# Performance work log

Hardware: AMD Instinct MI355X
Metric: run time of the kernel (lower is better)

Reference implementation:

```python
import jax, jax.numpy as jnp
import numpy as np

H, D_MODEL, DK, DV = 16, 1024, 64, 64
B, S = 4, 2048
LN_EPS = 1e-6
NEG = -1e9


def setup_inputs() -> dict:
    key = jax.random.key(0)
    ks = jax.random.split(key, 8)
    query = jax.random.normal(ks[0], (B, S, D_MODEL), dtype=jnp.float32)
    k_in = jax.random.normal(ks[1], (B, S, D_MODEL), dtype=jnp.float32)
    v_in = jax.random.normal(ks[2], (B, S, D_MODEL), dtype=jnp.float32)
    mask = jax.random.randint(ks[3], (B, S, S), 0, 2, dtype=jnp.int32)
    sc = 1.0 / np.sqrt(D_MODEL)
    w_qs = jax.random.normal(ks[4], (D_MODEL, H * DK), dtype=jnp.float32) * sc
    w_ks = jax.random.normal(ks[5], (D_MODEL, H * DK), dtype=jnp.float32) * sc
    w_vs = jax.random.normal(ks[6], (D_MODEL, H * DV), dtype=jnp.float32) * sc
    w_out = jax.random.normal(ks[7], (H * DV, D_MODEL), dtype=jnp.float32) * (1.0 / np.sqrt(H * DV))
    ln_g = jnp.ones((D_MODEL,), dtype=jnp.float32)
    ln_b = jnp.zeros((D_MODEL,), dtype=jnp.float32)
    return {"query": query, "key": k_in, "value": v_in, "mask": mask,
            "w_qs": w_qs, "w_ks": w_ks, "w_vs": w_vs, "w_out": w_out,
            "ln_g": ln_g, "ln_b": ln_b}


def reference(query, key, value, mask, w_qs, w_ks, w_vs, w_out, ln_g, ln_b):
    # projections -> [B, H, S, dk/dv]
    q = (query @ w_qs).reshape(B, S, H, DK).transpose(0, 2, 1, 3)
    k = (key @ w_ks).reshape(B, S, H, DK).transpose(0, 2, 1, 3)
    v = (value @ w_vs).reshape(B, S, H, DV).transpose(0, 2, 1, 3)
    scores = jnp.einsum('bhqd,bhkd->bhqk', q, k) / np.sqrt(DK)
    scores = jnp.where(mask[:, None, :, :] == 0, NEG, scores)
    p = jax.nn.softmax(scores, axis=-1)  # dropout = identity in eval
    x = jnp.einsum('bhqk,bhkd->bhqd', p, v)  # [B,H,S,DV]
    x = x.transpose(0, 2, 1, 3).reshape(B, S, H * DV)
    out = x @ w_out + query  # dropout identity, residual
    mu = out.mean(-1, keepdims=True)
    var = out.var(-1, keepdims=True)
    return (out - mu) / jnp.sqrt(var + LN_EPS) * ln_g + ln_b
```

## Files before the change

### kernel.cpp

```cpp
#include <hip/hip_runtime.h>

#define BB   4
#define SS   2048
#define HH   16
#define DM   1024
#define DKV  64
#define LNEPS 1e-6f

#define MD_BF16 0
#define MD_F32  1
#define MD_F16  2

typedef __attribute__((ext_vector_type(8))) short bf16x8;
typedef __attribute__((ext_vector_type(4))) float f32x4;
#define MFMA16(a,b,c) __builtin_amdgcn_mfma_f32_16x16x32_bf16(a,b,c,0,0,0)

__device__ __forceinline__ void gl_lds16(const ushort* g, ushort* l) {
    __builtin_amdgcn_global_load_lds(
        (const __attribute__((address_space(1))) void*)g,
        (__attribute__((address_space(3))) void*)l, 16, 0, 0);
}
__device__ __forceinline__ void wait_vm0_barrier() {
    asm volatile("s_waitcnt vmcnt(0)" ::: "memory");
    __builtin_amdgcn_s_barrier();
}

__device__ __forceinline__ float2 unpack2(unsigned int u) {
    union { unsigned int i; float f; } a, b;
    a.i = u << 16;
    b.i = u & 0xffff0000u;
    return make_float2(a.f, b.f);
}
__device__ __forceinline__ unsigned short f2bf(float f) {
    union { float f; unsigned int i; } c; c.f = f;
    unsigned int u = c.i;
    unsigned int r = u + 0x7fffu + ((u >> 16) & 1u);
    return (unsigned short)(r >> 16);
}
__device__ __forceinline__ unsigned short f2bf_t(float f) {
    union { float f; unsigned int i; } c; c.f = f;
    return (unsigned short)(c.i >> 16);
}
__device__ __forceinline__ float h2f(unsigned int bits16) {
    unsigned short s = (unsigned short)bits16;
    _Float16 x;
    __builtin_memcpy(&x, &s, 2);
    return (float)x;
}
__device__ __forceinline__ void load8m(const void* p, int mode, size_t e0, float* o) {
    if (mode == MD_F32) {
        const float* f = (const float*)p + e0;
        float4 a = *(const float4*)f;
        float4 b = *(const float4*)(f + 4);
        o[0] = a.x; o[1] = a.y; o[2] = a.z; o[3] = a.w;
        o[4] = b.x; o[5] = b.y; o[6] = b.z; o[7] = b.w;
    } else {
        uint4 u = *(const uint4*)((const ushort*)p + e0);
        unsigned v[4] = {u.x, u.y, u.z, u.w};
        if (mode == MD_BF16) {
#pragma unroll
            for (int j = 0; j < 4; ++j) { float2 t = unpack2(v[j]); o[2*j] = t.x; o[2*j+1] = t.y; }
        } else {
#pragma unroll
            for (int j = 0; j < 4; ++j) { o[2*j] = h2f(v[j] & 0xFFFFu); o[2*j+1] = h2f(v[j] >> 16); }
        }
    }
}
__device__ __forceinline__ void load4m(const void* p, int mode, size_t e0, float* o) {
    if (mode == MD_F32) {
        float4 v = *(const float4*)((const float*)p + e0);
        o[0] = v.x; o[1] = v.y; o[2] = v.z; o[3] = v.w;
    } else {
        uint2 u = *(const uint2*)((const ushort*)p + e0);
        if (mode == MD_BF16) {
            float2 a = unpack2(u.x), b = unpack2(u.y);
            o[0] = a.x; o[1] = a.y; o[2] = b.x; o[3] = b.y;
        } else {
            o[0] = h2f(u.x & 0xFFFFu); o[1] = h2f(u.x >> 16);
            o[2] = h2f(u.y & 0xFFFFu); o[3] = h2f(u.y >> 16);
        }
    }
}
__device__ __forceinline__ float loadS(const void* p, int mode, size_t i) {
    if (mode == MD_F32) return ((const float*)p)[i];
    unsigned short u = ((const ushort*)p)[i];
    if (mode == MD_BF16) { union { unsigned i; float f; } c; c.i = (unsigned)u << 16; return c.f; }
    return h2f(u);
}

struct SniffArgs { const void* p[10]; int nhalf[10]; };

__global__ void sniff_all(SniffArgs a, int* __restrict__ modes) {
    __shared__ int cE, cO;
    const int slots[9] = {0, 1, 2, 4, 5, 6, 7, 8, 9};
    const int slot = slots[blockIdx.x];
    const ushort* p = (const ushort*)a.p[slot];
    const int nhalf = a.nhalf[slot];
    if (threadIdx.x == 0) { cE = 0; cO = 0; }
    __syncthreads();
    int e = 0, o = 0;
    for (int i = threadIdx.x; i < nhalf; i += 256) {
        unsigned ex = (p[i] >> 7) & 0xFFu;
        int hit = (ex < 100u || ex == 0xFFu) ? 1 : 0;
        if (i & 1) o += hit; else e += hit;
    }
    atomicAdd(&cE, e);
    atomicAdd(&cO, o);
    __syncthreads();
    if (threadIdx.x == 0) {
        int total = cE + cO;
        modes[slot] = (total < 48) ? MD_BF16 : ((cO * 4 < cE) ? MD_F32 : MD_F16);
    }
}

__global__ __launch_bounds__(256) void mpack(
    const int* __restrict__ mask, unsigned int* __restrict__ pm)
{
    const int w = blockIdx.x * 256 + threadIdx.x;
    const int* p = mask + (size_t)w * 32;
    unsigned int bits = 0u;
#pragma unroll
    for (int j = 0; j < 8; ++j) {
        int4 v = *(const int4*)(p + j * 4);
        bits |= (v.x ? 1u : 0u) << (4 * j);
        bits |= (v.y ? 1u : 0u) << (4 * j + 1);
        bits |= (v.z ? 1u : 0u) << (4 * j + 2);
        bits |= (v.w ? 1u : 0u) << (4 * j + 3);
    }
    pm[w] = bits;
}

__global__ __launch_bounds__(256) void aconv(
    const void* __restrict__ A, ushort* __restrict__ Ab,
    const int* __restrict__ modes, int slot)
{
    const int m = modes[slot];
    const size_t e0 = ((size_t)blockIdx.x * 256 + threadIdx.x) * 16;
    float t[16];
    load8m(A, m, e0, t);
    load8m(A, m, e0 + 8, t + 8);
    union { ushort u[16]; uint4 v[2]; } p;
#pragma unroll
    for (int j = 0; j < 16; ++j) p.u[j] = f2bf(t[j]);
    *(uint4*)&Ab[e0]     = p.v[0];
    *(uint4*)&Ab[e0 + 8] = p.v[1];
}

struct WtArgs { const void* W[3]; ushort* Wt[3]; int slot[3]; };

__device__ __forceinline__ void wtrans_body(
    const void* __restrict__ W, ushort* __restrict__ Wt, int m)
{
    __shared__ ushort T[64][68];
    const int tid = threadIdx.x;
    const int k0 = blockIdx.y * 64, n0 = blockIdx.x * 64;

    const int r = tid >> 2, c = (tid & 3) * 16;
    float t[4];
#pragma unroll
    for (int j = 0; j < 4; ++j) {
        load4m(W, m, (size_t)(k0 + r) * DM + n0 + c + 4 * j, t);
#pragma unroll
        for (int i = 0; i < 4; ++i) T[r][c + 4 * j + i] = f2bf(t[i]);
    }
    __syncthreads();

    const int rn = tid >> 2, ck = (tid & 3) * 16;
    union { ushort u[8]; uint4 v; } p0, p1;
#pragma unroll
    for (int j = 0; j < 8; ++j) { p0.u[j] = T[ck + j][rn]; p1.u[j] = T[ck + 8 + j][rn]; }
    ushort* op = &Wt[(size_t)(n0 + rn) * DM + k0 + ck];
    *(uint4*)op = p0.v;
    *(uint4*)(op + 8) = p1.v;
}

__global__ __launch_bounds__(256) void wtrans3(WtArgs a, const int* __restrict__ modes) {
    const int g = blockIdx.z;
    wtrans_body(a.W[g], a.Wt[g], modes[a.slot[g]]);
}
__global__ __launch_bounds__(256) void wtrans(
    const void* __restrict__ W, ushort* __restrict__ Wt,
    const int* __restrict__ modes, int wslot)
{
    wtrans_body(W, Wt, modes[wslot]);
}

__global__ __launch_bounds__(256) void proj_mfma(
    const ushort* __restrict__ A, const ushort* __restrict__ Wt,
    ushort* __restrict__ Out, int vmode, float scale)
{
    __shared__ __align__(16) ushort Asf[2][4096];
    __shared__ __align__(16) ushort Bsf[2][4096];

    const int tid = threadIdx.x;
    const int lane = tid & 63, wv = tid >> 6;
    const int quad = lane >> 4, L = lane & 15;
    const int bid = blockIdx.y * gridDim.x + blockIdx.x;
    const int swz = (bid & 7) * 64 + (bid >> 3);
    const int m0 = (swz >> 3) * 128, n0 = (swz & 7) * 128;
    const int wm = (wv >> 1) * 64, wn = (wv & 1) * 64;

    const int e0 = (wv * 2 + 0) * 512 + lane * 8;
    const int e1 = (wv * 2 + 1) * 512 + lane * 8;
    const ushort* gA0 = A  + (size_t)(m0 + (e0 >> 5)) * DM + (e0 & 31);
    const ushort* gA1 = A  + (size_t)(m0 + (e1 >> 5)) * DM + (e1 & 31);
    const ushort* gB0 = Wt + (size_t)(n0 + (e0 >> 5)) * DM + (e0 & 31);
    const ushort* gB1 = Wt + (size_t)(n0 + (e1 >> 5)) * DM + (e1 & 31);

    f32x4 acc[4][4];
#pragma unroll
    for (int i = 0; i < 4; ++i)
#pragma unroll
        for (int j = 0; j < 4; ++j) { acc[i][j][0] = 0.f; acc[i][j][1] = 0.f; acc[i][j][2] = 0.f; acc[i][j][3] = 0.f; }

    gl_lds16(gA0, &Asf[0][e0]);
    gl_lds16(gA1, &Asf[0][e1]);
    gl_lds16(gB0, &Bsf[0][e0]);
    gl_lds16(gB1, &Bsf[0][e1]);
    wait_vm0_barrier();

    int cur = 0;
    for (int kt = 0; kt < 31; ++kt) {
        const int kn = (kt + 1) * 32;
        gl_lds16(gA0 + kn, &Asf[cur ^ 1][e0]);
        gl_lds16(gA1 + kn, &Asf[cur ^ 1][e1]);
        gl_lds16(gB0 + kn, &Bsf[cur ^ 1][e0]);
        gl_lds16(gB1 + kn, &Bsf[cur ^ 1][e1]);

        bf16x8 af[4], bfr[4];
#pragma unroll
        for (int tm = 0; tm < 4; ++tm) af[tm] = *(const bf16x8*)&Asf[cur][(wm + tm * 16 + L) * 32 + quad * 8];
#pragma unroll
        for (int tn = 0; tn < 4; ++tn) bfr[tn] = *(const bf16x8*)&Bsf[cur][(wn + tn * 16 + L) * 32 + quad * 8];
#pragma unroll
        for (int tm = 0; tm < 4; ++tm)
#pragma unroll
            for (int tn = 0; tn < 4; ++tn)
                acc[tm][tn] = MFMA16(af[tm], bfr[tn], acc[tm][tn]);

        wait_vm0_barrier();
        cur ^= 1;
    }
    {
        bf16x8 af[4], bfr[4];
#pragma unroll
        for (int tm = 0; tm < 4; ++tm) af[tm] = *(const bf16x8*)&Asf[cur][(wm + tm * 16 + L) * 32 + quad * 8];
#pragma unroll
        for (int tn = 0; tn < 4; ++tn) bfr[tn] = *(const bf16x8*)&Bsf[cur][(wn + tn * 16 + L) * 32 + quad * 8];
#pragma unroll
        for (int tm = 0; tm < 4; ++tm)
#pragma unroll
            for (int tn = 0; tn < 4; ++tn)
                acc[tm][tn] = MFMA16(af[tm], bfr[tn], acc[tm][tn]);
    }

#pragma unroll
    for (int tm = 0; tm < 4; ++tm)
#pragma unroll
        for (int tn = 0; tn < 4; ++tn)
#pragma unroll
            for (int r = 0; r < 4; ++r) {
                const int mm = m0 + wm + tm * 16 + quad * 4 + r;
                const int n = n0 + wn + tn * 16 + L;
                const int b = mm >> 11, s = mm & 2047;
                const int h = n >> 6, d = n & 63;
                const size_t o = vmode
                    ? ((size_t)(b * HH + h) * DKV + d) * SS + s
                    : ((size_t)(b * HH + h) * SS + s) * DKV + d;
                Out[o] = f2bf(acc[tm][tn][r] * scale);
            }
}

__global__ __launch_bounds__(256) void attn_mfma(
    const ushort* __restrict__ Q, const ushort* __restrict__ K,
    const ushort* __restrict__ Vt, const unsigned int* __restrict__ pm,
    ushort* __restrict__ Xo)
{
    __shared__ __align__(16) ushort Ks[64][72];
    __shared__ __align__(16) ushort Vs[64][72];
    __shared__ __align__(16) ushort Ps[64][72];

    const int tid = threadIdx.x;
    const int lane = tid & 63, wv = tid >> 6;
    const int quad = lane >> 4, L = lane & 15;
    const int bid = blockIdx.y * gridDim.x + blockIdx.x;
    const int swz = (bid & 7) * 256 + (bid >> 3);
    const int bh = swz >> 5, b = bh >> 4, h = bh & 15;
    const int q0 = (swz & 31) * 64;

    const ushort* qp = &Q[((size_t)bh * SS + q0 + wv * 16 + L) * DKV + quad * 8];
    const bf16x8 aq0 = *(const bf16x8*)qp;
    const bf16x8 aq1 = *(const bf16x8*)(qp + 32);

    f32x4 O[4];
    float lacc[4];
#pragma unroll
    for (int t = 0; t < 4; ++t) { O[t][0] = 0.f; O[t][1] = 0.f; O[t][2] = 0.f; O[t][3] = 0.f; }
#pragma unroll
    for (int r = 0; r < 4; ++r) lacc[r] = 0.f;

    const int sr = tid >> 2, sg = tid & 3;
    const ushort* kbase = &K[((size_t)bh * SS + sr) * DKV + sg * 16];
    const ushort* vbase = &Vt[((size_t)bh * DKV + sr) * SS + sg * 16];
    const unsigned int* pmr[4];
#pragma unroll
    for (int r = 0; r < 4; ++r)
        pmr[r] = pm + ((size_t)b * SS + q0 + wv * 16 + quad * 4 + r) * 64;

    for (int kt = 0; kt < 32; ++kt) {
        __syncthreads();
        *(uint4*)&Ks[sr][sg * 16]     = *(const uint4*)kbase;
        *(uint4*)&Ks[sr][sg * 16 + 8] = *(const uint4*)(kbase + 8);
        *(uint4*)&Vs[sr][sg * 16]     = *(const uint4*)vbase;
        *(uint4*)&Vs[sr][sg * 16 + 8] = *(const uint4*)(vbase + 8);
        kbase += 64 * DKV;
        vbase += 64;

        uint2 mw[4];
#pragma unroll
        for (int r = 0; r < 4; ++r) mw[r] = *(const uint2*)(pmr[r] + 2 * kt);

        __syncthreads();

        f32x4 sc[4];
        __builtin_amdgcn_s_setprio(1);
#pragma unroll
        for (int t = 0; t < 4; ++t) {
            bf16x8 b0 = *(const bf16x8*)&Ks[t * 16 + L][quad * 8];
            bf16x8 b1 = *(const bf16x8*)&Ks[t * 16 + L][32 + quad * 8];
            f32x4 c; c[0] = 0.f; c[1] = 0.f; c[2] = 0.f; c[3] = 0.f;
            c = MFMA16(aq0, b0, c);
            c = MFMA16(aq1, b1, c);
            sc[t] = c;
        }
        __builtin_amdgcn_s_setprio(0);

#pragma unroll
        for (int r = 0; r < 4; ++r) {
            const unsigned mx = mw[r].x, my = mw[r].y;
#pragma unroll
            for (int t = 0; t < 4; ++t) {
                const float s = fminf(sc[t][r], 30.f);
                const float e = __expf(s);
                const unsigned wsel = (t & 2) ? my : mx;
                const float p = ((wsel >> ((t & 1) * 16 + L)) & 1u) ? e : 0.f;
                lacc[r] += p;
                Ps[wv * 16 + quad * 4 + r][t * 16 + L] = f2bf_t(p);
            }
        }

        bf16x8 ap0 = *(const bf16x8*)&Ps[wv * 16 + L][quad * 8];
        bf16x8 ap1 = *(const bf16x8*)&Ps[wv * 16 + L][32 + quad * 8];
        __builtin_amdgcn_s_setprio(1);
#pragma unroll
        for (int t = 0; t < 4; ++t) {
            bf16x8 v0 = *(const bf16x8*)&Vs[t * 16 + L][quad * 8];
            bf16x8 v1 = *(const bf16x8*)&Vs[t * 16 + L][32 + quad * 8];
            O[t] = MFMA16(ap0, v0, O[t]);
            O[t] = MFMA16(ap1, v1, O[t]);
        }
        __builtin_amdgcn_s_setprio(0);
    }

    float inv[4];
#pragma unroll
    for (int r = 0; r < 4; ++r) {
        float l = lacc[r];
#pragma unroll
        for (int off = 1; off < 16; off <<= 1) l += __shfl_xor(l, off, 64);
        inv[r] = 1.f / l;
    }
#pragma unroll
    for (int t = 0; t < 4; ++t)
#pragma unroll
        for (int r = 0; r < 4; ++r) {
            const int qg = q0 + wv * 16 + quad * 4 + r;
            Xo[((size_t)b * SS + qg) * DM + h * DKV + t * 16 + L] = f2bf(O[t][r] * inv[r]);
        }
}

__global__ __launch_bounds__(256) void oproj_mfma(
    const ushort* __restrict__ Xin, const ushort* __restrict__ Wt,
    const void* __restrict__ Qres, float* __restrict__ Out,
    const int* __restrict__ modes)
{
    __shared__ __align__(16) ushort Asf[2][4096];
    __shared__ __align__(16) ushort Bsf[2][4096];

    const int tid = threadIdx.x;
    const int lane = tid & 63, wv = tid >> 6;
    const int quad = lane >> 4, L = lane & 15;
    const int bid = blockIdx.y * gridDim.x + blockIdx.x;
    const int swz = (bid & 7) * 64 + (bid >> 3);
    const int m0 = (swz >> 3) * 128, n0 = (swz & 7) * 128;
    const int wm = (wv >> 1) * 64, wn = (wv & 1) * 64;
    const int mq = modes[0];

    const int e0 = (wv * 2 + 0) * 512 + lane * 8;
    const int e1 = (wv * 2 + 1) * 512 + lane * 8;
    const ushort* gA0 = Xin + (size_t)(m0 + (e0 >> 5)) * DM + (e0 & 31);
    const ushort* gA1 = Xin + (size_t)(m0 + (e1 >> 5)) * DM + (e1 & 31);
    const ushort* gB0 = Wt  + (size_t)(n0 + (e0 >> 5)) * DM + (e0 & 31);
    const ushort* gB1 = Wt  + (size_t)(n0 + (e1 >> 5)) * DM + (e1 & 31);

    f32x4 acc[4][4];
#pragma unroll
    for (int i = 0; i < 4; ++i)
#pragma unroll
        for (int j = 0; j < 4; ++j) { acc[i][j][0] = 0.f; acc[i][j][1] = 0.f; acc[i][j][2] = 0.f; acc[i][j][3] = 0.f; }

    gl_lds16(gA0, &Asf[0][e0]);
    gl_lds16(gA1, &Asf[0][e1]);
    gl_lds16(gB0, &Bsf[0][e0]);
    gl_lds16(gB1, &Bsf[0][e1]);
    wait_vm0_barrier();

    int cur = 0;
    for (int kt = 0; kt < 31; ++kt) {
        const int kn = (kt + 1) * 32;
        gl_lds16(gA0 + kn, &Asf[cur ^ 1][e0]);
        gl_lds16(gA1 + kn, &Asf[cur ^ 1][e1]);
        gl_lds16(gB0 + kn, &Bsf[cur ^ 1][e0]);
        gl_lds16(gB1 + kn, &Bsf[cur ^ 1][e1]);

        bf16x8 af[4], bfr[4];
#pragma unroll
        for (int tm = 0; tm < 4; ++tm) af[tm] = *(const bf16x8*)&Asf[cur][(wm + tm * 16 + L) * 32 + quad * 8];
#pragma unroll
        for (int tn = 0; tn < 4; ++tn) bfr[tn] = *(const bf16x8*)&Bsf[cur][(wn + tn * 16 + L) * 32 + quad * 8];
#pragma unroll
        for (int tm = 0; tm < 4; ++tm)
#pragma unroll
            for (int tn = 0; tn < 4; ++tn)
                acc[tm][tn] = MFMA16(af[tm], bfr[tn], acc[tm][tn]);

        wait_vm0_barrier();
        cur ^= 1;
    }
    {
        bf16x8 af[4], bfr[4];
#pragma unroll
        for (int tm = 0; tm < 4; ++tm) af[tm] = *(const bf16x8*)&Asf[cur][(wm + tm * 16 + L) * 32 + quad * 8];
#pragma unroll
        for (int tn = 0; tn < 4; ++tn) bfr[tn] = *(const bf16x8*)&Bsf[cur][(wn + tn * 16 + L) * 32 + quad * 8];
#pragma unroll
        for (int tm = 0; tm < 4; ++tm)
#pragma unroll
            for (int tn = 0; tn < 4; ++tn)
                acc[tm][tn] = MFMA16(af[tm], bfr[tn], acc[tm][tn]);
    }

#pragma unroll
    for (int tm = 0; tm < 4; ++tm)
#pragma unroll
        for (int tn = 0; tn < 4; ++tn)
#pragma unroll
            for (int r = 0; r < 4; ++r) {
                const int mm = m0 + wm + tm * 16 + quad * 4 + r;
                const int n = n0 + wn + tn * 16 + L;
                const size_t idx = (size_t)mm * DM + n;
                Out[idx] = acc[tm][tn][r] + loadS(Qres, mq, idx);
            }
}

__global__ __launch_bounds__(256) void ln_k(
    float* __restrict__ Out, const void* __restrict__ G,
    const void* __restrict__ Bt, const int* __restrict__ modes)
{
    const int tid = threadIdx.x, wv = tid >> 6, lane = tid & 63;
    const int row = blockIdx.x * 4 + wv;
    const int mg = modes[8], mb = modes[9];
    const size_t base = (size_t)row * DM + lane * 16;

    float v[16];
    float s = 0.f, q = 0.f;
#pragma unroll
    for (int j = 0; j < 16; j += 4) {
        float4 t = *(const float4*)&Out[base + j];
        v[j] = t.x; v[j+1] = t.y; v[j+2] = t.z; v[j+3] = t.w;
        s += t.x + t.y + t.z + t.w;
        q += t.x*t.x + t.y*t.y + t.z*t.z + t.w*t.w;
    }
#pragma unroll
    for (int off = 1; off < 64; off <<= 1) {
        s += __shfl_xor(s, off, 64);
        q += __shfl_xor(q, off, 64);
    }
    const float mu = s * (1.f / 1024.f);
    const float var = q * (1.f / 1024.f) - mu * mu;
    const float inv = rsqrtf(var + LNEPS);

    float gj[16], bj[16];
#pragma unroll
    for (int j = 0; j < 16; j += 4) {
        load4m(G,  mg, (size_t)lane * 16 + j, gj + j);
        load4m(Bt, mb, (size_t)lane * 16 + j, bj + j);
    }
#pragma unroll
    for (int j = 0; j < 16; j += 4) {
        float4 o;
        o.x = (v[j]   - mu) * inv * gj[j]   + bj[j];
        o.y = (v[j+1] - mu) * inv * gj[j+1] + bj[j+1];
        o.z = (v[j+2] - mu) * inv * gj[j+2] + bj[j+2];
        o.w = (v[j+3] - mu) * inv * gj[j+3] + bj[j+3];
        *(float4*)&Out[base + j] = o;
    }
}

extern "C" void kernel_launch(void* const* d_in, const int* in_sizes, int n_in,
                              void* d_out, int out_size, void* d_ws, size_t ws_size,
                              hipStream_t stream)
{
    const void* query = d_in[0];
    const void* key_i = d_in[1];
    const void* value = d_in[2];
    const int*  mask  = (const int*)d_in[3];
    const void* w_qs  = d_in[4];
    const void* w_ks  = d_in[5];
    const void* w_vs  = d_in[6];
    const void* w_out = d_in[7];
    const void* ln_g  = d_in[8];
    const void* ln_b  = d_in[9];
    float* out = (float*)d_out;

    int* modes = (int*)d_ws;
    const size_t PE = (size_t)BB * HH * SS * DKV;
    ushort* Qw = (ushort*)((char*)d_ws + 256);
    ushort* Kw = Qw + PE;
    ushort* Vw = Kw + PE;
    ushort* Xw = Vw + PE;
    ushort* Abuf = Xw;
    ushort* Wtq  = (ushort*)((char*)d_out + (4  << 20));
    ushort* Wtk  = (ushort*)((char*)d_out + (8  << 20));
    ushort* Wtv  = (ushort*)((char*)d_out + (12 << 20));
    ushort* Wt2  = Qw;
    unsigned int* pmask = (unsigned int*)d_out;

    SniffArgs sa;
    for (int i = 0; i < 10; ++i) {
        sa.p[i] = d_in[i];
        sa.nhalf[i] = in_sizes[i] < 4096 ? in_sizes[i] : 4096;
    }
    sniff_all<<<9, 256, 0, stream>>>(sa, modes);
    mpack<<<2048, 256, 0, stream>>>(mask, pmask);

    WtArgs wa;
    wa.W[0] = w_qs; wa.Wt[0] = Wtq; wa.slot[0] = 4;
    wa.W[1] = w_ks; wa.Wt[1] = Wtk; wa.slot[1] = 5;
    wa.W[2] = w_vs; wa.Wt[2] = Wtv; wa.slot[2] = 6;
    wtrans3<<<dim3(16, 16, 3), 256, 0, stream>>>(wa, modes);

    dim3 gproj(8, 64), gtr(16, 16);

    aconv<<<2048, 256, 0, stream>>>(query, Abuf, modes, 0);
    proj_mfma<<<gproj, 256, 0, stream>>>(Abuf, Wtq, Qw, 0, 0.125f);

    aconv<<<2048, 256, 0, stream>>>(key_i, Abuf, modes, 1);
    proj_mfma<<<gproj, 256, 0, stream>>>(Abuf, Wtk, Kw, 0, 1.0f);

    aconv<<<2048, 256, 0, stream>>>(value, Abuf, modes, 2);
    proj_mfma<<<gproj, 256, 0, stream>>>(Abuf, Wtv, Vw, 1, 1.0f);

    attn_mfma<<<dim3(32, 64), 256, 0, stream>>>(Qw, Kw, Vw, pmask, Xw);

    wtrans<<<gtr, 256, 0, stream>>>(w_out, Wt2, modes, 7);
    oproj_mfma<<<gproj, 256, 0, stream>>>(Xw, Wt2, query, out, modes);
    ln_k<<<2048, 256, 0, stream>>>(out, ln_g, ln_b, modes);
}
```

Measured before the change: 527.1 us.

## Fuse prep kernels, batch Q/V projections, and load V fragments directly

Merges mask packing, all weight transposes, and query/value bf16 conversion into one prep launch. Dtype sniffing now runs inside each consumer block instead of in a separate kernel. Q and V projections share one launch via a z dimension. Attention reads V fragments straight from global memory instead of staging them in LDS. Oproj writes to a workspace buffer and layernorm writes the final output. Together these cut launches and serial dependencies, at the cost of redundant per-block sniffing and uncoalesced V loads.

```diff
diff --git a/kernel.cpp b/kernel.cpp
--- a/kernel.cpp
+++ b/kernel.cpp
@@ -46,25 +46,6 @@
     _Float16 x;
     __builtin_memcpy(&x, &s, 2);
     return (float)x;
-}
-__device__ __forceinline__ void load8m(const void* p, int mode, size_t e0, float* o) {
-    if (mode == MD_F32) {
-        const float* f = (const float*)p + e0;
-        float4 a = *(const float4*)f;
-        float4 b = *(const float4*)(f + 4);
-        o[0] = a.x; o[1] = a.y; o[2] = a.z; o[3] = a.w;
-        o[4] = b.x; o[5] = b.y; o[6] = b.z; o[7] = b.w;
-    } else {
-        uint4 u = *(const uint4*)((const ushort*)p + e0);
-        unsigned v[4] = {u.x, u.y, u.z, u.w};
-        if (mode == MD_BF16) {
-#pragma unroll
-            for (int j = 0; j < 4; ++j) { float2 t = unpack2(v[j]); o[2*j] = t.x; o[2*j+1] = t.y; }
-        } else {
-#pragma unroll
-            for (int j = 0; j < 4; ++j) { o[2*j] = h2f(v[j] & 0xFFFFu); o[2*j+1] = h2f(v[j] >> 16); }
-        }
-    }
 }
 __device__ __forceinline__ void load4m(const void* p, int mode, size_t e0, float* o) {
     if (mode == MD_F32) {
@@ -88,14 +69,38 @@
     return h2f(u);
 }
 
-struct SniffArgs { const void* p[10]; int nhalf[10]; };
-
-__global__ void sniff_all(SniffArgs a, int* __restrict__ modes) {
+__device__ __forceinline__ void loadAraw(const void* p, int m, size_t e, uint4* r) {
+    if (m == MD_F32) {
+        const float* f = (const float*)p + e;
+        r[0] = *(const uint4*)(f);
+        r[1] = *(const uint4*)(f + 4);
+        r[2] = *(const uint4*)(f + 8);
+        r[3] = *(const uint4*)(f + 12);
+    } else {
+        const ushort* s = (const ushort*)p + e;
+        r[0] = *(const uint4*)s;
+        r[1] = *(const uint4*)(s + 8);
+    }
+}
+__device__ __forceinline__ void cvtA16(const uint4* r, int m, uint4* o2) {
+    union { ushort u[16]; uint4 v[2]; } o;
+    if (m == MD_F32) {
+        const float* f = (const float*)r;
+#pragma unroll
+        for (int j = 0; j < 16; ++j) o.u[j] = f2bf(f[j]);
+    } else if (m == MD_BF16) {
+        o.v[0] = r[0]; o.v[1] = r[1];
+    } else {
+        const ushort* s = (const ushort*)r;
+#pragma unroll
+        for (int j = 0; j < 16; ++j) o.u[j] = f2bf(h2f(s[j]));
+    }
+    o2[0] = o.v[0]; o2[1] = o.v[1];
+}
+
+__device__ __forceinline__ int sniff_local(const void* p_, int nhalf) {
     __shared__ int cE, cO;
-    const int slots[9] = {0, 1, 2, 4, 5, 6, 7, 8, 9};
-    const int slot = slots[blockIdx.x];
-    const ushort* p = (const ushort*)a.p[slot];
-    const int nhalf = a.nhalf[slot];
+    const ushort* p = (const ushort*)p_;
     if (threadIdx.x == 0) { cE = 0; cO = 0; }
     __syncthreads();
     int e = 0, o = 0;
@@ -107,53 +112,16 @@
     atomicAdd(&cE, e);
     atomicAdd(&cO, o);
     __syncthreads();
-    if (threadIdx.x == 0) {
-        int total = cE + cO;
-        modes[slot] = (total < 48) ? MD_BF16 : ((cO * 4 < cE) ? MD_F32 : MD_F16);
-    }
-}
-
-__global__ __launch_bounds__(256) void mpack(
-    const int* __restrict__ mask, unsigned int* __restrict__ pm)
-{
-    const int w = blockIdx.x * 256 + threadIdx.x;
-    const int* p = mask + (size_t)w * 32;
-    unsigned int bits = 0u;
-#pragma unroll
-    for (int j = 0; j < 8; ++j) {
-        int4 v = *(const int4*)(p + j * 4);
-        bits |= (v.x ? 1u : 0u) << (4 * j);
-        bits |= (v.y ? 1u : 0u) << (4 * j + 1);
-        bits |= (v.z ? 1u : 0u) << (4 * j + 2);
-        bits |= (v.w ? 1u : 0u) << (4 * j + 3);
-    }
-    pm[w] = bits;
-}
-
-__global__ __launch_bounds__(256) void aconv(
-    const void* __restrict__ A, ushort* __restrict__ Ab,
-    const int* __restrict__ modes, int slot)
-{
-    const int m = modes[slot];
-    const size_t e0 = ((size_t)blockIdx.x * 256 + threadIdx.x) * 16;
-    float t[16];
-    load8m(A, m, e0, t);
-    load8m(A, m, e0 + 8, t + 8);
-    union { ushort u[16]; uint4 v[2]; } p;
-#pragma unroll
-    for (int j = 0; j < 16; ++j) p.u[j] = f2bf(t[j]);
-    *(uint4*)&Ab[e0]     = p.v[0];
-    *(uint4*)&Ab[e0 + 8] = p.v[1];
-}
-
-struct WtArgs { const void* W[3]; ushort* Wt[3]; int slot[3]; };
+    const int total = cE + cO;
+    return (total < 48) ? MD_BF16 : ((cO * 4 < cE) ? MD_F32 : MD_F16);
+}
 
 __device__ __forceinline__ void wtrans_body(
-    const void* __restrict__ W, ushort* __restrict__ Wt, int m)
+    const void* __restrict__ W, ushort* __restrict__ Wt, int m, int sub)
 {
     __shared__ ushort T[64][68];
     const int tid = threadIdx.x;
-    const int k0 = blockIdx.y * 64, n0 = blockIdx.x * 64;
+    const int n0 = (sub & 15) * 64, k0 = (sub >> 4) * 64;
 
     const int r = tid >> 2, c = (tid & 3) * 16;
     float t[4];
@@ -174,23 +142,76 @@
     *(uint4*)(op + 8) = p1.v;
 }
 
-__global__ __launch_bounds__(256) void wtrans3(WtArgs a, const int* __restrict__ modes) {
-    const int g = blockIdx.z;
-    wtrans_body(a.W[g], a.Wt[g], modes[a.slot[g]]);
-}
-__global__ __launch_bounds__(256) void wtrans(
-    const void* __restrict__ W, ushort* __restrict__ Wt,
-    const int* __restrict__ modes, int wslot)
-{
-    wtrans_body(W, Wt, modes[wslot]);
-}
-
-__global__ __launch_bounds__(256) void proj_mfma(
-    const ushort* __restrict__ A, const ushort* __restrict__ Wt,
-    ushort* __restrict__ Out, int vmode, float scale)
+__device__ __forceinline__ void aconv_body(
+    const void* __restrict__ A, ushort* __restrict__ Ab, int bidl)
+{
+    const int m = sniff_local(A, 4096);
+    const size_t e0 = ((size_t)bidl * 256 + threadIdx.x) * 16;
+    uint4 r[4], o[2];
+    loadAraw(A, m, e0, r);
+    cvtA16(r, m, o);
+    *(uint4*)&Ab[e0]     = o[0];
+    *(uint4*)&Ab[e0 + 8] = o[1];
+}
+
+__global__ __launch_bounds__(256) void prep(
+    const int* __restrict__ mask, unsigned int* __restrict__ pm,
+    const void* __restrict__ w_qs, const void* __restrict__ w_ks,
+    const void* __restrict__ w_vs, const void* __restrict__ w_out,
+    ushort* __restrict__ Wtq, ushort* __restrict__ Wtk,
+    ushort* __restrict__ Wtv, ushort* __restrict__ Wt2,
+    const void* __restrict__ query, const void* __restrict__ value,
+    ushort* __restrict__ Abq, ushort* __restrict__ Abv)
+{
+    const int bid = blockIdx.x;
+    if (bid < 2048) {
+        const int w = bid * 256 + threadIdx.x;
+        const int* p = mask + (size_t)w * 32;
+        unsigned int bits = 0u;
+#pragma unroll
+        for (int j = 0; j < 8; ++j) {
+            int4 v = *(const int4*)(p + j * 4);
+            bits |= (v.x ? 1u : 0u) << (4 * j);
+            bits |= (v.y ? 1u : 0u) << (4 * j + 1);
+            bits |= (v.z ? 1u : 0u) << (4 * j + 2);
+            bits |= (v.w ? 1u : 0u) << (4 * j + 3);
+        }
+        pm[w] = bits;
+    } else if (bid < 3072) {
+        const int b2 = bid - 2048;
+        const int g = b2 >> 8, sub = b2 & 255;
+        const void* W = (g == 0) ? w_qs : (g == 1) ? w_ks : (g == 2) ? w_vs : w_out;
+        ushort* Wt = (g == 0) ? Wtq : (g == 1) ? Wtk : (g == 2) ? Wtv : Wt2;
+        wtrans_body(W, Wt, sniff_local(W, 4096), sub);
+    } else if (bid < 5120) {
+        aconv_body(query, Abq, bid - 3072);
+    } else {
+        aconv_body(value, Abv, bid - 5120);
+    }
+}
+
+__global__ __launch_bounds__(256) void aconv_k(
+    const void* __restrict__ A, ushort* __restrict__ Ab)
+{
+    aconv_body(A, Ab, blockIdx.x);
+}
+
+struct ProjArgs {
+    const ushort* A[2]; const ushort* Wt[2]; ushort* Out[2];
+    int vmode[2]; float scale[2];
+};
+
+__global__ __launch_bounds__(256) void proj_mfma(ProjArgs pa)
 {
     __shared__ __align__(16) ushort Asf[2][4096];
     __shared__ __align__(16) ushort Bsf[2][4096];
+
+    const int z = blockIdx.z;
+    const ushort* A  = pa.A[z];
+    const ushort* Wt = pa.Wt[z];
+    ushort* Out = pa.Out[z];
+    const int vmode = pa.vmode[z];
+    const float scale = pa.scale[z];
 
     const int tid = threadIdx.x;
     const int lane = tid & 63, wv = tid >> 6;
@@ -277,7 +298,6 @@
     ushort* __restrict__ Xo)
 {
     __shared__ __align__(16) ushort Ks[64][72];
-    __shared__ __align__(16) ushort Vs[64][72];
     __shared__ __align__(16) ushort Ps[64][72];
 
     const int tid = threadIdx.x;
@@ -301,7 +321,10 @@
 
     const int sr = tid >> 2, sg = tid & 3;
     const ushort* kbase = &K[((size_t)bh * SS + sr) * DKV + sg * 16];
-    const ushort* vbase = &Vt[((size_t)bh * DKV + sr) * SS + sg * 16];
+    const ushort* vb[4];
+#pragma unroll
+    for (int t = 0; t < 4; ++t)
+        vb[t] = &Vt[((size_t)bh * DKV + t * 16 + L) * SS + quad * 8];
     const unsigned int* pmr[4];
 #pragma unroll
     for (int r = 0; r < 4; ++r)
@@ -311,10 +334,15 @@
         __syncthreads();
         *(uint4*)&Ks[sr][sg * 16]     = *(const uint4*)kbase;
         *(uint4*)&Ks[sr][sg * 16 + 8] = *(const uint4*)(kbase + 8);
-        *(uint4*)&Vs[sr][sg * 16]     = *(const uint4*)vbase;
-        *(uint4*)&Vs[sr][sg * 16 + 8] = *(const uint4*)(vbase + 8);
         kbase += 64 * DKV;
-        vbase += 64;
+
+        bf16x8 vf0[4], vf1[4];
+#pragma unroll
+        for (int t = 0; t < 4; ++t) {
+            vf0[t] = *(const bf16x8*)(vb[t]);
+            vf1[t] = *(const bf16x8*)(vb[t] + 32);
+            vb[t] += 64;
+        }
 
         uint2 mw[4];
 #pragma unroll
@@ -354,10 +382,8 @@
         __builtin_amdgcn_s_setprio(1);
 #pragma unroll
         for (int t = 0; t < 4; ++t) {
-            bf16x8 v0 = *(const bf16x8*)&Vs[t * 16 + L][quad * 8];
-            bf16x8 v1 = *(const bf16x8*)&Vs[t * 16 + L][32 + quad * 8];
-            O[t] = MFMA16(ap0, v0, O[t]);
-            O[t] = MFMA16(ap1, v1, O[t]);
+            O[t] = MFMA16(ap0, vf0[t], O[t]);
+            O[t] = MFMA16(ap1, vf1[t], O[t]);
         }
         __builtin_amdgcn_s_setprio(0);
     }
@@ -381,11 +407,12 @@
 
 __global__ __launch_bounds__(256) void oproj_mfma(
     const ushort* __restrict__ Xin, const ushort* __restrict__ Wt,
-    const void* __restrict__ Qres, float* __restrict__ Out,
-    const int* __restrict__ modes)
+    const void* __restrict__ Qres, float* __restrict__ OutF)
 {
     __shared__ __align__(16) ushort Asf[2][4096];
     __shared__ __align__(16) ushort Bsf[2][4096];
+
+    const int mq = sniff_local(Qres, 4096);
 
     const int tid = threadIdx.x;
     const int lane = tid & 63, wv = tid >> 6;
@@ -394,7 +421,6 @@
     const int swz = (bid & 7) * 64 + (bid >> 3);
     const int m0 = (swz >> 3) * 128, n0 = (swz & 7) * 128;
     const int wm = (wv >> 1) * 64, wn = (wv & 1) * 64;
-    const int mq = modes[0];
 
     const int e0 = (wv * 2 + 0) * 512 + lane * 8;
     const int e1 = (wv * 2 + 1) * 512 + lane * 8;
@@ -459,24 +485,26 @@
                 const int mm = m0 + wm + tm * 16 + quad * 4 + r;
                 const int n = n0 + wn + tn * 16 + L;
                 const size_t idx = (size_t)mm * DM + n;
-                Out[idx] = acc[tm][tn][r] + loadS(Qres, mq, idx);
+                OutF[idx] = acc[tm][tn][r] + loadS(Qres, mq, idx);
             }
 }
 
 __global__ __launch_bounds__(256) void ln_k(
-    float* __restrict__ Out, const void* __restrict__ G,
-    const void* __restrict__ Bt, const int* __restrict__ modes)
-{
+    const float* __restrict__ In, float* __restrict__ Out,
+    const void* __restrict__ G, const void* __restrict__ Bt)
+{
+    const int mg = sniff_local(G, 1024);
+    const int mb = sniff_local(Bt, 1024);
+
     const int tid = threadIdx.x, wv = tid >> 6, lane = tid & 63;
     const int row = blockIdx.x * 4 + wv;
-    const int mg = modes[8], mb = modes[9];
     const size_t base = (size_t)row * DM + lane * 16;
 
     float v[16];
     float s = 0.f, q = 0.f;
 #pragma unroll
     for (int j = 0; j < 16; j += 4) {
-        float4 t = *(const float4*)&Out[base + j];
+        float4 t = *(const float4*)&In[base + j];
         v[j] = t.x; v[j+1] = t.y; v[j+2] = t.z; v[j+3] = t.w;
         s += t.x + t.y + t.z + t.w;
         q += t.x*t.x + t.y*t.y + t.z*t.z + t.w*t.w;
@@ -523,47 +551,39 @@
     const void* ln_b  = d_in[9];
     float* out = (float*)d_out;
 
-    int* modes = (int*)d_ws;
     const size_t PE = (size_t)BB * HH * SS * DKV;
     ushort* Qw = (ushort*)((char*)d_ws + 256);
     ushort* Kw = Qw + PE;
     ushort* Vw = Kw + PE;
     ushort* Xw = Vw + PE;
-    ushort* Abuf = Xw;
-    ushort* Wtq  = (ushort*)((char*)d_out + (4  << 20));
-    ushort* Wtk  = (ushort*)((char*)d_out + (8  << 20));
-    ushort* Wtv  = (ushort*)((char*)d_out + (12 << 20));
-    ushort* Wt2  = Qw;
+    float*  OutF = (float*)Qw;
     unsigned int* pmask = (unsigned int*)d_out;
-
-    SniffArgs sa;
-    for (int i = 0; i < 10; ++i) {
-        sa.p[i] = d_in[i];
-        sa.nhalf[i] = in_sizes[i] < 4096 ? in_sizes[i] : 4096;
-    }
-    sniff_all<<<9, 256, 0, stream>>>(sa, modes);
-    mpack<<<2048, 256, 0, stream>>>(mask, pmask);
-
-    WtArgs wa;
-    wa.W[0] = w_qs; wa.Wt[0] = Wtq; wa.slot[0] = 4;
-    wa.W[1] = w_ks; wa.Wt[1] = Wtk; wa.slot[1] = 5;
-    wa.W[2] = w_vs; wa.Wt[2] = Wtv; wa.slot[2] = 6;
-    wtrans3<<<dim3(16, 16, 3), 256, 0, stream>>>(wa, modes);
-
-    dim3 gproj(8, 64), gtr(16, 16);
-
-    aconv<<<2048, 256, 0, stream>>>(query, Abuf, modes, 0);
-    proj_mfma<<<gproj, 256, 0, stream>>>(Abuf, Wtq, Qw, 0, 0.125f);
-
-    aconv<<<2048, 256, 0, stream>>>(key_i, Abuf, modes, 1);
-    proj_mfma<<<gproj, 256, 0, stream>>>(Abuf, Wtk, Kw, 0, 1.0f);
-
-    aconv<<<2048, 256, 0, stream>>>(value, Abuf, modes, 2);
-    proj_mfma<<<gproj, 256, 0, stream>>>(Abuf, Wtv, Vw, 1, 1.0f);
+    ushort* Wtq = (ushort*)((char*)d_out + (2 << 20));
+    ushort* Wtk = (ushort*)((char*)d_out + (4 << 20));
+    ushort* Wtv = (ushort*)((char*)d_out + (6 << 20));
+    ushort* Wt2 = (ushort*)((char*)d_out + (8 << 20));
+    ushort* Abq = (ushort*)((char*)d_out + (10 << 20));
+    ushort* Abv = Xw;
+    ushort* Abk = Xw;
+
+    prep<<<7168, 256, 0, stream>>>(mask, pmask, w_qs, w_ks, w_vs, w_out,
+                                   Wtq, Wtk, Wtv, Wt2, query, value, Abq, Abv);
+
+    ProjArgs pqv;
+    pqv.A[0] = Abq; pqv.Wt[0] = Wtq; pqv.Out[0] = Qw; pqv.vmode[0] = 0; pqv.scale[0] = 0.125f;
+    pqv.A[1] = Abv; pqv.Wt[1] = Wtv; pqv.Out[1] = Vw; pqv.vmode[1] = 1; pqv.scale[1] = 1.0f;
+    proj_mfma<<<dim3(8, 64, 2), 256, 0, stream>>>(pqv);
+
+    aconv_k<<<2048, 256, 0, stream>>>(key_i, Abk);
+
+    ProjArgs pk;
+    pk.A[0] = Abk; pk.Wt[0] = Wtk; pk.Out[0] = Kw; pk.vmode[0] = 0; pk.scale[0] = 1.0f;
+    pk.A[1] = Abk; pk.Wt[1] = Wtk; pk.Out[1] = Kw; pk.vmode[1] = 0; pk.scale[1] = 1.0f;
+    proj_mfma<<<dim3(8, 64, 1), 256, 0, stream>>>(pk);
 
     attn_mfma<<<dim3(32, 64), 256, 0, stream>>>(Qw, Kw, Vw, pmask, Xw);
 
-    wtrans<<<gtr, 256, 0, stream>>>(w_out, Wt2, modes, 7);
-    oproj_mfma<<<gproj, 256, 0, stream>>>(Xw, Wt2, query, out, modes);
-    ln_k<<<2048, 256, 0, stream>>>(out, ln_g, ln_b, modes);
-}
+    oproj_mfma<<<dim3(8, 64), 256, 0, stream>>>(Xw, Wt2, query, OutF);
+
+    ln_k<<<2048, 256, 0, stream>>>(OutF, out, ln_g, ln_b);
+}
```

Measured after the change: 691.9 us. 1.31x slower.
